# Kernel tuning notes

Hardware: AMD Instinct MI355X
Metric: run time of the kernel (lower is better)

## Reference

```python
import jax, jax.numpy as jnp
import numpy as np

N_LAYERS = 2
H = 16                      # num_heads
ARW = (1.0, 1.0)            # att_residual_weight
MCB = (0.0, 1.0)            # mask_clip_balancer
LN_EPS = 1e-5


def _ln(x, g, b):
    mu = jnp.mean(x, axis=-1, keepdims=True)
    var = jnp.mean(jnp.square(x - mu), axis=-1, keepdims=True)
    return (x - mu) * jax.lax.rsqrt(var + LN_EPS) * g + b


def _quick_gelu(u):
    return u * jax.nn.sigmoid(1.702 * u)


def setup_inputs() -> dict:
    key = jax.random.key(0)
    ks = jax.random.split(key, 8)
    L, B, C = 577, 8, 1024
    d_ff = 4 * C
    inp = {
        'x': jax.random.normal(ks[0], (L, B, C), jnp.float32),
        'att_bias': jax.random.normal(ks[1], (N_LAYERS, B * H, L, L), jnp.float32),
        'ln1_g': jnp.ones((N_LAYERS, C), jnp.float32),
        'ln1_b': jnp.zeros((N_LAYERS, C), jnp.float32),
        'in_w': 0.02 * jax.random.normal(ks[2], (N_LAYERS, 3 * C, C), jnp.float32),
        'in_b': jnp.zeros((N_LAYERS, 3 * C), jnp.float32),
        'out_w': 0.02 * jax.random.normal(ks[3], (N_LAYERS, C, C), jnp.float32),
        'out_b': jnp.zeros((N_LAYERS, C), jnp.float32),
        'ln2_g': jnp.ones((N_LAYERS, C), jnp.float32),
        'ln2_b': jnp.zeros((N_LAYERS, C), jnp.float32),
        'fc1_w': 0.02 * jax.random.normal(ks[4], (N_LAYERS, d_ff, C), jnp.float32),
        'fc1_b': jnp.zeros((N_LAYERS, d_ff), jnp.float32),
        'fc2_w': 0.02 * jax.random.normal(ks[5], (N_LAYERS, C, d_ff), jnp.float32),
        'fc2_b': jnp.zeros((N_LAYERS, C), jnp.float32),
    }
    return inp


def reference(x, att_bias, ln1_g, ln1_b, in_w, in_b, out_w, out_b,
              ln2_g, ln2_b, fc1_w, fc1_b, fc2_w, fc2_b):
    L, B, C = x.shape
    d = C // H
    scale = d ** -0.5  # custom_att_factor is None
    for i in range(N_LAYERS):
        # --- custom CSA attention ---
        h = _ln(x, ln1_g[i], ln1_b[i])                              # [L,B,C]
        qkv = jnp.einsum('lbc,fc->lbf', h, in_w[i]) + in_b[i]       # [L,B,3C]
        q, k, v = jnp.split(qkv, 3, axis=-1)
        to_heads = lambda t: t.reshape(L, B, H, d).transpose(1, 2, 0, 3)  # [B,H,L,d]
        q, k, v = to_heads(q), to_heads(k), to_heads(v)
        bias = att_bias[i].reshape(B, H, L, L)
        q_attn = bias + scale * jnp.einsum('bhld,bhmd->bhlm', q, q)
        k_attn = bias + scale * jnp.einsum('bhld,bhmd->bhlm', k, k)
        attn = jax.nn.softmax(q_attn, axis=-1) + jax.nn.softmax(k_attn, axis=-1)
        attn = attn * 0.5                                           # norm_att=True
        attn = jnp.mean(attn, axis=1, keepdims=True)                # avg_att=True -> [B,1,L,L]
        out = jnp.matmul(attn, v)                                   # broadcast over H -> [B,H,L,d]
        out = MCB[0] * v + MCB[1] * out
        out = out.transpose(2, 0, 1, 3).reshape(L, B, C)
        out = jnp.einsum('lbc,oc->lbo', out, out_w[i]) + out_b[i]
        x = ARW[0] * x + ARW[1] * out
        # --- MLP residual ---
        h2 = _ln(x, ln2_g[i], ln2_b[i])
        u = _quick_gelu(jnp.einsum('lbc,fc->lbf', h2, fc1_w[i]) + fc1_b[i])
        x = x + jnp.einsum('lbf,cf->lbc', u, fc2_w[i]) + fc2_b[i]
    return x
```

## Files before the change

kernel.cpp:

```cpp
#include <hip/hip_runtime.h>

typedef float f32x4 __attribute__((ext_vector_type(4)));
typedef __bf16 bf16x8 __attribute__((ext_vector_type(8)));

#define L_SEQ 577
#define BB 8
#define CC 1024
#define HH 16
#define ROWS (L_SEQ*BB)

static __device__ __forceinline__ ushort f2b(float f) {
  unsigned u = __float_as_uint(f);
  u += 0x7fffu + ((u >> 16) & 1u);
  return (ushort)(u >> 16);
}

static __device__ __forceinline__ void gld16(const void* g, void* l) {
  __builtin_amdgcn_global_load_lds((const __attribute__((address_space(1))) void*)g,
                                   (__attribute__((address_space(3))) void*)l, 16, 0, 0);
}

__global__ void cvt4_kernel(const float* __restrict__ s0, ushort* __restrict__ d0, int n0,
                            const float* __restrict__ s1, ushort* __restrict__ d1, int n1,
                            const float* __restrict__ s2, ushort* __restrict__ d2, int n2,
                            const float* __restrict__ s3, ushort* __restrict__ d3, int n3)
{
  int i = blockIdx.x * blockDim.x + threadIdx.x;
  const float* src; ushort* dst;
  if (i < n0)                { src = s0; dst = d0; }
  else if ((i -= n0) < n1)   { src = s1; dst = d1; }
  else if ((i -= n1) < n2)   { src = s2; dst = d2; }
  else if ((i -= n2) < n3)   { src = s3; dst = d3; }
  else return;
  float4 v = *(const float4*)(src + (size_t)i * 4);
  ushort4 o;
  o.x = f2b(v.x); o.y = f2b(v.y); o.z = f2b(v.z); o.w = f2b(v.w);
  *(ushort4*)(dst + (size_t)i * 4) = o;
}

template<int NP, bool DOLN>
__global__ __launch_bounds__(256)
void ln_resid_kernel(const float* __restrict__ xsrc, const float* __restrict__ parts,
                     const float* __restrict__ cbias,
                     const float* __restrict__ g, const float* __restrict__ be,
                     float* __restrict__ xdst, ushort* __restrict__ hout)
{
  const int row = blockIdx.x;
  const int t = threadIdx.x;
  float4 v = *(const float4*)(xsrc + (size_t)row * CC + t * 4);
  if (NP > 0) {
    float4 c4 = *(const float4*)(cbias + t * 4);
    v.x += c4.x; v.y += c4.y; v.z += c4.z; v.w += c4.w;
    #pragma unroll
    for (int p = 0; p < NP; ++p) {
      float4 pv = *(const float4*)(parts + ((size_t)p * ROWS + row) * CC + t * 4);
      v.x += pv.x; v.y += pv.y; v.z += pv.z; v.w += pv.w;
    }
  }
  *(float4*)(xdst + (size_t)row * CC + t * 4) = v;
  if (DOLN) {
    float s  = v.x + v.y + v.z + v.w;
    float s2 = v.x*v.x + v.y*v.y + v.z*v.z + v.w*v.w;
    #pragma unroll
    for (int sd = 1; sd < 64; sd <<= 1) { s += __shfl_xor(s, sd, 64); s2 += __shfl_xor(s2, sd, 64); }
    __shared__ float ps[4], ps2[4];
    const int w = t >> 6;
    if ((t & 63) == 0) { ps[w] = s; ps2[w] = s2; }
    __syncthreads();
    s  = ps[0] + ps[1] + ps[2] + ps[3];
    s2 = ps2[0] + ps2[1] + ps2[2] + ps2[3];
    const float mean = s * (1.f / 1024.f);
    const float var  = s2 * (1.f / 1024.f) - mean * mean;
    const float rstd = rsqrtf(var + 1e-5f);
    float4 gv = *(const float4*)(g + t * 4);
    float4 bv = *(const float4*)(be + t * 4);
    ushort4 o;
    o.x = f2b((v.x - mean) * rstd * gv.x + bv.x);
    o.y = f2b((v.y - mean) * rstd * gv.y + bv.y);
    o.z = f2b((v.z - mean) * rstd * gv.z + bv.z);
    o.w = f2b((v.w - mean) * rstd * gv.w + bv.w);
    *(ushort4*)(hout + (size_t)row * CC + t * 4) = o;
  }
}

__global__ __launch_bounds__(256)
void vt_kernel(const ushort* __restrict__ qkv, ushort* __restrict__ vt)
{
  __shared__ ushort tile[32][33];
  const int lt = blockIdx.x * 32;
  const int nt = blockIdx.y * 32;
  const int b  = blockIdx.z;
  const int tx = threadIdx.x & 31;
  const int ty = threadIdx.x >> 5;
  #pragma unroll
  for (int p = 0; p < 4; ++p) {
    int l = lt + ty + p * 8;
    ushort v = 0;
    if (l < L_SEQ) v = qkv[((size_t)l * BB + b) * 3072 + 2048 + nt + tx];
    tile[ty + p * 8][tx] = v;
  }
  __syncthreads();
  #pragma unroll
  for (int p = 0; p < 4; ++p) {
    int n = nt + ty + p * 8;
    int l = lt + tx;
    vt[((size_t)b * 1024 + n) * 608 + l] = tile[tx][ty + p * 8];
  }
}

__global__ __launch_bounds__(512, 2)
void attn_kernel(const ushort* __restrict__ qkv,
                 const float* __restrict__ bias,
                 ushort* __restrict__ attnp)
{
  __shared__ float2 red[2][2][8][16];
  __shared__ ushort sm[32][612];
  const int t = threadIdx.x;
  const int lane = t & 63;
  const int w = t >> 6;
  const int fr = lane & 15;
  const int lq = lane >> 4;
  const int id = blockIdx.x;
  const int b  = id & 7;
  const int rem = id >> 3;
  const int rb = rem % 19;
  const int hg = rem / 19;
  const int r0 = rb * 32;
  const int kc = lq * 8;

  int rowl[2]; size_t rbase[2];
  #pragma unroll
  for (int rs = 0; rs < 2; ++rs) {
    rowl[rs] = min(r0 + rs * 16 + fr, L_SEQ - 1);
    rbase[rs] = ((size_t)rowl[rs] * BB + b) * 3072;
  }
  size_t cbs_[5]; int c0_[5];
  #pragma unroll
  for (int it = 0; it < 5; ++it) {
    const int nt = w + it * 8;
    const int crow = min(nt * 16 + fr, L_SEQ - 1);
    cbs_[it] = ((size_t)crow * BB + b) * 3072;
    c0_[it] = nt * 16 + lq * 4;
  }

  float acc[2][5][4];
  #pragma unroll
  for (int rs = 0; rs < 2; ++rs)
    #pragma unroll
    for (int it = 0; it < 5; ++it)
      #pragma unroll
      for (int r = 0; r < 4; ++r) acc[rs][it][r] = 0.f;

  for (int h4 = 0; h4 < 4; ++h4) {
    const int h = hg * 4 + h4;
    const float* brow0 = bias + (((size_t)(b * HH + h)) * L_SEQ + rowl[0]) * L_SEQ;
    const float* brow1 = bias + (((size_t)(b * HH + h)) * L_SEQ + rowl[1]) * L_SEQ;
    float bs[2][5][4];
    #pragma unroll
    for (int it = 0; it < 5; ++it)
      #pragma unroll
      for (int r = 0; r < 4; ++r) {
        const int cc = min(c0_[it] + r, L_SEQ - 1);
        bs[0][it][r] = brow0[cc];
        bs[1][it][r] = brow1[cc];
      }
    #pragma unroll
    for (int v = 0; v < 2; ++v) {
      const int off = (v ? CC : 0) + h * 64;
      bf16x8 rf0[2], rf1[2];
      #pragma unroll
      for (int rs = 0; rs < 2; ++rs) {
        rf0[rs] = *(const bf16x8*)(qkv + rbase[rs] + off + kc);
        rf1[rs] = *(const bf16x8*)(qkv + rbase[rs] + off + 32 + kc);
      }
      bf16x8 cA0 = *(const bf16x8*)(qkv + cbs_[0] + off + kc);
      bf16x8 cA1 = *(const bf16x8*)(qkv + cbs_[0] + off + 32 + kc);
      bf16x8 cB0 = *(const bf16x8*)(qkv + cbs_[1] + off + kc);
      bf16x8 cB1 = *(const bf16x8*)(qkv + cbs_[1] + off + 32 + kc);
      float s[2][5][4];
      #pragma unroll
      for (int it = 0; it < 5; ++it) {
        const bf16x8 c0f = cA0, c1f = cA1;
        cA0 = cB0; cA1 = cB1;
        if (it + 2 < 5) {
          cB0 = *(const bf16x8*)(qkv + cbs_[it + 2] + off + kc);
          cB1 = *(const bf16x8*)(qkv + cbs_[it + 2] + off + 32 + kc);
        }
        f32x4 d0 = {0.f, 0.f, 0.f, 0.f};
        f32x4 d1 = {0.f, 0.f, 0.f, 0.f};
        d0 = __builtin_amdgcn_mfma_f32_16x16x32_bf16(c0f, rf0[0], d0, 0, 0, 0);
        d0 = __builtin_amdgcn_mfma_f32_16x16x32_bf16(c1f, rf1[0], d0, 0, 0, 0);
        d1 = __builtin_amdgcn_mfma_f32_16x16x32_bf16(c0f, rf0[1], d1, 0, 0, 0);
        d1 = __builtin_amdgcn_mfma_f32_16x16x32_bf16(c1f, rf1[1], d1, 0, 0, 0);
        #pragma unroll
        for (int r = 0; r < 4; ++r) {
          const bool cv = (c0_[it] + r < L_SEQ);
          s[0][it][r] = cv ? (bs[0][it][r] + 0.125f * d0[r]) : -1e30f;
          s[1][it][r] = cv ? (bs[1][it][r] + 0.125f * d1[r]) : -1e30f;
        }
      }
      float mw[2], sw[2];
      #pragma unroll
      for (int rs = 0; rs < 2; ++rs) {
        float m = -1e30f;
        #pragma unroll
        for (int it = 0; it < 5; ++it)
          #pragma unroll
          for (int r = 0; r < 4; ++r) m = fmaxf(m, s[rs][it][r]);
        m = fmaxf(m, __shfl_xor(m, 16, 64));
        m = fmaxf(m, __shfl_xor(m, 32, 64));
        float sum = 0.f;
        #pragma unroll
        for (int it = 0; it < 5; ++it)
          #pragma unroll
          for (int r = 0; r < 4; ++r) { s[rs][it][r] = __expf(s[rs][it][r] - m); sum += s[rs][it][r]; }
        sum += __shfl_xor(sum, 16, 64);
        sum += __shfl_xor(sum, 32, 64);
        mw[rs] = m; sw[rs] = sum;
      }
      const int p = (h4 * 2 + v) & 1;
      if (lane < 16) {
        red[p][0][w][lane] = make_float2(mw[0], sw[0]);
        red[p][1][w][lane] = make_float2(mw[1], sw[1]);
      }
      __syncthreads();
      #pragma unroll
      for (int rs = 0; rs < 2; ++rs) {
        float m = -1e30f;
        #pragma unroll
        for (int ww = 0; ww < 8; ++ww) m = fmaxf(m, red[p][rs][ww][fr].x);
        float smm = 0.f;
        #pragma unroll
        for (int ww = 0; ww < 8; ++ww) {
          const float2 q = red[p][rs][ww][fr];
          smm += q.y * __expf(q.x - m);
        }
        const float f = 0.03125f * __expf(mw[rs] - m) / smm;
        #pragma unroll
        for (int it = 0; it < 5; ++it)
          #pragma unroll
          for (int r = 0; r < 4; ++r) acc[rs][it][r] += s[rs][it][r] * f;
      }
    }
  }

  #pragma unroll
  for (int rs = 0; rs < 2; ++rs)
    #pragma unroll
    for (int it = 0; it < 5; ++it) {
      if (c0_[it] < 608) {
        ushort4 o;
        o.x = f2b(acc[rs][it][0]); o.y = f2b(acc[rs][it][1]);
        o.z = f2b(acc[rs][it][2]); o.w = f2b(acc[rs][it][3]);
        *(ushort4*)&sm[rs * 16 + fr][c0_[it]] = o;
      }
    }
  __syncthreads();
  ushort* dst = attnp + ((size_t)hg * 8 + b) * 608 * 608 + (size_t)r0 * 608;
  for (int j = t; j < 32 * 152; j += 512) {
    const int row = j / 152;
    const int c4 = (j % 152) * 4;
    if (r0 + row < L_SEQ)
      *(ushort4*)(dst + (size_t)row * 608 + c4) = *(const ushort4*)&sm[row][c4];
  }
}

__global__ __launch_bounds__(256)
void attn_combine(const ushort* __restrict__ attnp, ushort* __restrict__ attn)
{
  const int t = threadIdx.x;
  if (t >= 152) return;
  const int l = blockIdx.x;
  const int b = blockIdx.y;
  const int c0 = t * 4;
  const size_t base = ((size_t)b * 608 + l) * 608 + c0;
  const size_t hs = (size_t)8 * 608 * 608;
  float s[4] = {0.f, 0.f, 0.f, 0.f};
  #pragma unroll
  for (int p = 0; p < 4; ++p) {
    ushort4 v = *(const ushort4*)(attnp + p * hs + base);
    s[0] += __uint_as_float((unsigned)v.x << 16);
    s[1] += __uint_as_float((unsigned)v.y << 16);
    s[2] += __uint_as_float((unsigned)v.z << 16);
    s[3] += __uint_as_float((unsigned)v.w << 16);
  }
  ushort4 o;
  const bool lv = (l < L_SEQ);
  o.x = (lv && c0 + 0 < L_SEQ) ? f2b(s[0]) : (ushort)0;
  o.y = (lv && c0 + 1 < L_SEQ) ? f2b(s[1]) : (ushort)0;
  o.z = (lv && c0 + 2 < L_SEQ) ? f2b(s[2]) : (ushort)0;
  o.w = (lv && c0 + 3 < L_SEQ) ? f2b(s[3]) : (ushort)0;
  *(ushort4*)(attn + base) = o;
}

__global__ __launch_bounds__(256, 2)
void av_gemm(const ushort* __restrict__ A, int lda, int Arows, long aStride,
             const ushort* __restrict__ B, int ldb, long bStride,
             int M, int K,
             ushort* __restrict__ outb, int ldo)
{
  __shared__ __align__(16) ushort As[128 * 32];
  __shared__ __align__(16) ushort Bs[128 * 32];
  const int t = threadIdx.x;
  const int lane = t & 63;
  const int w = t >> 6;
  const int bm = blockIdx.x, bn = blockIdx.y, bz = blockIdx.z;
  const ushort* Ab = A + (long)bz * aStride;
  const ushort* Bb = B + (long)bz * bStride;
  const int srow = t >> 2;
  const int sc = (t & 3) * 8;
  const int wr = (w >> 1) * 64;
  const int wc = (w & 1) * 64;
  const int am1 = Arows - 1;
  f32x4 acc[4][4] = {};

  const int r0a = bm * 128 + srow;
  const int r0b = bn * 128 + srow;
  for (int kt = 0; kt < K; kt += 32) {
    __syncthreads();
    gld16(Ab + (size_t)min(r0a, am1) * lda + kt + sc, (void*)(As + t * 8));
    gld16(Ab + (size_t)min(r0a + 64, am1) * lda + kt + sc, (void*)(As + 2048 + t * 8));
    gld16(Bb + (size_t)r0b * ldb + kt + sc, (void*)(Bs + t * 8));
    gld16(Bb + (size_t)(r0b + 64) * ldb + kt + sc, (void*)(Bs + 2048 + t * 8));
    asm volatile("s_waitcnt vmcnt(0)" ::: "memory");
    __syncthreads();
    bf16x8 av[4], bv[4];
    const int fr = lane & 15;
    const int kc = (lane >> 4) * 8;
    #pragma unroll
    for (int m = 0; m < 4; ++m) av[m] = *(const bf16x8*)(As + (wr + m * 16 + fr) * 32 + kc);
    #pragma unroll
    for (int n = 0; n < 4; ++n) bv[n] = *(const bf16x8*)(Bs + (wc + n * 16 + fr) * 32 + kc);
    #pragma unroll
    for (int m = 0; m < 4; ++m)
      #pragma unroll
      for (int n = 0; n < 4; ++n)
        acc[m][n] = __builtin_amdgcn_mfma_f32_16x16x32_bf16(av[m], bv[n], acc[m][n], 0, 0, 0);
  }
  const int rbase = wr + (lane >> 4) * 4;
  const int cbase = wc + (lane & 15);
  #pragma unroll
  for (int n = 0; n < 4; ++n) {
    const int gn = bn * 128 + cbase + n * 16;
    #pragma unroll
    for (int m = 0; m < 4; ++m) {
      f32x4 d = acc[m][n];
      #pragma unroll
      for (int r = 0; r < 4; ++r) {
        const int gm = bm * 128 + rbase + m * 16 + r;
        if (gm < M) outb[((size_t)gm * 8 + bz) * ldo + gn] = f2b(d[r]);
      }
    }
  }
}

#define RD_A8(BOFS, MH) \
  _Pragma("unroll") for (int ks = 0; ks < 2; ++ks) \
  _Pragma("unroll") for (int m = 0; m < 4; ++m) \
    Af[ks][m] = rdA(BOFS, MH, ks, m);

#define RD_B4(BOFS, NH) \
  _Pragma("unroll") for (int ks = 0; ks < 2; ++ks) \
  _Pragma("unroll") for (int n = 0; n < 2; ++n) \
    Bf[NH][ks][n] = rdB(BOFS, NH, ks, n);

#define MFQ(MH, NH) \
  _Pragma("unroll") for (int ks = 0; ks < 2; ++ks) \
  _Pragma("unroll") for (int m = 0; m < 4; ++m) \
  _Pragma("unroll") for (int n = 0; n < 2; ++n) \
    acc[(MH)*4+m][(NH)*2+n] = __builtin_amdgcn_mfma_f32_16x16x32_bf16( \
        Af[ks][m], Bf[NH][ks][n], acc[(MH)*4+m][(NH)*2+n], 0, 0, 0);

#define BARO() \
  __builtin_amdgcn_sched_barrier(0); \
  __builtin_amdgcn_s_barrier(); \
  asm volatile("s_waitcnt lgkmcnt(0)" ::: "memory"); \
  __builtin_amdgcn_sched_barrier(0); \
  __builtin_amdgcn_s_setprio(1);

#define MF_END() \
  __builtin_amdgcn_s_setprio(0); \
  __builtin_amdgcn_sched_barrier(0); \
  __builtin_amdgcn_s_barrier();

template<int EPI>
__global__ __launch_bounds__(512, 2)
void gemm8(const ushort* __restrict__ Ap, int lda, int Arows,
           const ushort* __restrict__ Bp, int ldb,
           int M, int Ksplit,
           const float* __restrict__ bias,
           ushort* __restrict__ outb, float* __restrict__ outf, int ldo)
{
  __shared__ __align__(16) char smem[131072];
  const int t = threadIdx.x;
  const int lane = t & 63;
  const int w = t >> 6;
  const int wm = w >> 2, wn = w & 3;
  const int gx = gridDim.x;
  const int nwg = gx * gridDim.y;
  int id = blockIdx.y * gx + blockIdx.x;
  {
    const int q8 = nwg >> 3, r8 = nwg & 7;
    const int xcd = id & 7, pos = id >> 3;
    id = (xcd < r8 ? xcd * (q8 + 1) : r8 * (q8 + 1) + (xcd - r8) * q8) + pos;
  }
  const int bm = id % gx, bn = id / gx;
  const int bz = blockIdx.z;
  const int k0 = bz * Ksplit;
  const int iters = Ksplit >> 7;
  const int fr = lane & 15, lq = lane >> 4;

  f32x4 acc[8][4] = {};
  bf16x8 Af[2][4];
  bf16x8 Bf[2][2][2];

  const int rowj0 = t >> 3,        cbj0 = t & 7;
  const int rowj1 = (t + 512) >> 3, cbj1 = (t + 512) & 7;
  const ushort* pA[2][2]; const ushort* pB[2][2];
  #pragma unroll
  for (int h = 0; h < 2; ++h) {
    pA[h][0] = Ap + (size_t)min(bm*256 + h*128 + rowj0, Arows-1) * lda + k0 + ((cbj0 ^ (rowj0 & 7)) << 3);
    pA[h][1] = Ap + (size_t)min(bm*256 + h*128 + rowj1, Arows-1) * lda + k0 + ((cbj1 ^ (rowj1 & 7)) << 3);
    pB[h][0] = Bp + (size_t)(bn*256 + h*128 + rowj0) * ldb + k0 + ((cbj0 ^ (rowj0 & 7)) << 3);
    pB[h][1] = Bp + (size_t)(bn*256 + h*128 + rowj1) * ldb + k0 + ((cbj1 ^ (rowj1 & 7)) << 3);
  }

  auto stA = [&](int kt, int bofs, int h) {
    gld16(pA[h][0] + kt * 64, smem + bofs + h * 16384 + t * 16);
    gld16(pA[h][1] + kt * 64, smem + bofs + h * 16384 + (t + 512) * 16);
  };
  auto stB = [&](int kt, int bofs, int h) {
    gld16(pB[h][0] + kt * 64, smem + bofs + 32768 + h * 16384 + t * 16);
    gld16(pB[h][1] + kt * 64, smem + bofs + 32768 + h * 16384 + (t + 512) * 16);
  };
  auto rdA = [&](int bofs, int mh, int ks, int m) -> bf16x8 {
    const int rl = wm * 64 + m * 16 + fr;
    const int cb = (ks * 4 + lq) ^ (fr & 7);
    return *(const bf16x8*)(smem + bofs + mh * 16384 + rl * 128 + cb * 16);
  };
  auto rdB = [&](int bofs, int nh, int ks, int n) -> bf16x8 {
    const int rl = wn * 32 + n * 16 + fr;
    const int cb = (ks * 4 + lq) ^ (fr & 7);
    return *(const bf16x8*)(smem + bofs + 32768 + nh * 16384 + rl * 128 + cb * 16);
  };

  stA(0, 0, 0); stB(0, 0, 0); stB(0, 0, 1); stA(0, 0, 1);
  stA(1, 65536, 0); stB(1, 65536, 1); stA(1, 65536, 1);
  asm volatile("s_waitcnt vmcnt(6)" ::: "memory");
  __builtin_amdgcn_sched_barrier(0);
  __builtin_amdgcn_s_barrier();

  for (int i = 0; i < iters; ++i) {
    const bool more = (i + 1 < iters);
    const int kt2 = 2 * i + 2;
    RD_A8(0, 0) RD_B4(0, 0)
    stB(2 * i + 1, 65536, 0);
    BARO(); MFQ(0, 0) MF_END();
    RD_B4(0, 1)
    if (more) stA(kt2, 0, 0);
    BARO(); MFQ(0, 1) MF_END();
    RD_A8(0, 1)
    if (more) stB(kt2, 0, 1);
    BARO(); MFQ(1, 1) MF_END();
    if (more) stA(kt2, 0, 1);
    BARO(); MFQ(1, 0)
    __builtin_amdgcn_s_setprio(0);
    if (more) { asm volatile("s_waitcnt vmcnt(6)" ::: "memory"); }
    else      { asm volatile("s_waitcnt vmcnt(0)" ::: "memory"); }
    __builtin_amdgcn_sched_barrier(0);
    __builtin_amdgcn_s_barrier();
    RD_A8(65536, 0) RD_B4(65536, 0)
    if (more) stB(kt2, 0, 0);
    BARO(); MFQ(0, 0) MF_END();
    RD_B4(65536, 1)
    if (more) stA(2 * i + 3, 65536, 0);
    BARO(); MFQ(0, 1) MF_END();
    RD_A8(65536, 1)
    if (more) stB(2 * i + 3, 65536, 1);
    BARO(); MFQ(1, 1) MF_END();
    if (more) stA(2 * i + 3, 65536, 1);
    BARO(); MFQ(1, 0)
    __builtin_amdgcn_s_setprio(0);
    if (more) { asm volatile("s_waitcnt vmcnt(6)" ::: "memory"); }
    __builtin_amdgcn_sched_barrier(0);
    __builtin_amdgcn_s_barrier();
  }

  #pragma unroll
  for (int mh = 0; mh < 2; ++mh)
  #pragma unroll
  for (int nh = 0; nh < 2; ++nh)
  #pragma unroll
  for (int n = 0; n < 2; ++n) {
    const int gn = bn * 256 + nh * 128 + wn * 32 + n * 16 + fr;
    const float bval = (EPI == 4) ? 0.f : bias[gn];
    #pragma unroll
    for (int m = 0; m < 4; ++m) {
      f32x4 d = acc[mh * 4 + m][nh * 2 + n];
      #pragma unroll
      for (int r = 0; r < 4; ++r) {
        const int gm = bm * 256 + mh * 128 + wm * 64 + m * 16 + lq * 4 + r;
        if (gm < M) {
          if (EPI == 0) {
            outb[(size_t)gm * ldo + gn] = f2b(d[r] + bval);
          } else if (EPI == 1) {
            float v0 = d[r] + bval;
            outb[(size_t)gm * ldo + gn] = f2b(v0 / (1.f + __expf(-1.702f * v0)));
          } else {
            outf[((size_t)bz * M + gm) * ldo + gn] = d[r];
          }
        }
      }
    }
  }
}

extern "C" void kernel_launch(void* const* d_in, const int* in_sizes, int n_in,
                              void* d_out, int out_size, void* d_ws, size_t ws_size,
                              hipStream_t stream)
{
  (void)in_sizes; (void)n_in; (void)out_size; (void)ws_size;
  const float* x_in  = (const float*)d_in[0];
  const float* attb  = (const float*)d_in[1];
  const float* ln1_g = (const float*)d_in[2];
  const float* ln1_b = (const float*)d_in[3];
  const float* in_w  = (const float*)d_in[4];
  const float* in_b  = (const float*)d_in[5];
  const float* out_w = (const float*)d_in[6];
  const float* out_b = (const float*)d_in[7];
  const float* ln2_g = (const float*)d_in[8];
  const float* ln2_b = (const float*)d_in[9];
  const float* fc1_w = (const float*)d_in[10];
  const float* fc1_b = (const float*)d_in[11];
  const float* fc2_w = (const float*)d_in[12];
  const float* fc2_b = (const float*)d_in[13];
  float* x = (float*)d_out;

  char* ws = (char*)d_ws;
  size_t off = 0;
  auto alloc = [&](size_t bytes) -> void* {
    void* p = ws + off; off += (bytes + 255) & ~(size_t)255; return p;
  };
  ushort* wIn   = (ushort*)alloc(2ull * 3072 * 1024 * 2);
  ushort* wOut  = (ushort*)alloc(2ull * 1024 * 1024 * 2);
  ushort* wF1   = (ushort*)alloc(2ull * 4096 * 1024 * 2);
  ushort* wF2   = (ushort*)alloc(2ull * 4096 * 1024 * 2);
  ushort* hbuf  = (ushort*)alloc((size_t)ROWS * 1024 * 2);
  ushort* qkv   = (ushort*)alloc((size_t)ROWS * 3072 * 2);
  ushort* vt    = (ushort*)alloc((size_t)8 * 1024 * 608 * 2);
  ushort* attn  = (ushort*)alloc((size_t)8 * 608 * 608 * 2);
  ushort* attnp = (ushort*)alloc((size_t)4 * 8 * 608 * 608 * 2);
  ushort* outlb = (ushort*)alloc((size_t)ROWS * 1024 * 2);
  float*  pbuf  = (float*)alloc((size_t)4 * ROWS * 1024 * 4);
  ushort* ubuf  = qkv;

  cvt4_kernel<<<(1572864 + 524288 + 2097152 + 2097152 + 255) / 256, 256, 0, stream>>>(
      in_w,  wIn,  1572864,
      out_w, wOut, 524288,
      fc1_w, wF1,  2097152,
      fc2_w, wF2,  2097152);
  ln_resid_kernel<0, true><<<ROWS, 256, 0, stream>>>(x_in, nullptr, nullptr,
      ln1_g, ln1_b, x, hbuf);

  for (int i = 0; i < 2; ++i) {
    gemm8<0><<<dim3(19, 12, 1), 512, 0, stream>>>(hbuf, 1024, ROWS,
        wIn + (size_t)i * 3072 * 1024, 1024,
        ROWS, 1024, in_b + i * 3072, qkv, nullptr, 3072);
    attn_kernel<<<dim3(608, 1, 1), 512, 0, stream>>>(qkv, attb + (size_t)i * 128 * 577 * 577, attnp);
    vt_kernel<<<dim3(19, 32, 8), 256, 0, stream>>>(qkv, vt);
    attn_combine<<<dim3(608, 8), 256, 0, stream>>>(attnp, attn);
    av_gemm<<<dim3(5, 8, 8), 256, 0, stream>>>(attn, 608, 577, (long)608 * 608,
        vt, 608, (long)1024 * 608, 577, 608, outlb, 1024);
    gemm8<4><<<dim3(19, 4, 2), 512, 0, stream>>>(outlb, 1024, ROWS,
        wOut + (size_t)i * 1024 * 1024, 1024,
        ROWS, 512, nullptr, nullptr, pbuf, 1024);
    ln_resid_kernel<2, true><<<ROWS, 256, 0, stream>>>(x, pbuf, out_b + i * 1024,
        ln2_g + i * 1024, ln2_b + i * 1024, x, hbuf);
    gemm8<1><<<dim3(19, 16, 1), 512, 0, stream>>>(hbuf, 1024, ROWS,
        wF1 + (size_t)i * 4096 * 1024, 1024,
        ROWS, 1024, fc1_b + i * 4096, ubuf, nullptr, 4096);
    gemm8<4><<<dim3(19, 4, 4), 512, 0, stream>>>(ubuf, 4096, ROWS,
        wF2 + (size_t)i * 4096 * 1024, 4096,
        ROWS, 1024, nullptr, nullptr, pbuf, 1024);
    if (i == 0) {
      ln_resid_kernel<4, true><<<ROWS, 256, 0, stream>>>(x, pbuf, fc2_b,
          ln1_g + 1024, ln1_b + 1024, x, hbuf);
    } else {
      ln_resid_kernel<4, false><<<ROWS, 256, 0, stream>>>(x, pbuf, fc2_b + 1024,
          nullptr, nullptr, x, nullptr);
    }
  }
}
```

Before: 998.3 us.

## Write Q and K head-major from the QKV GEMM epilogue for the attention kernel

The QKV projection GEMM gets a new epilogue that scatters Q and K into padded per-(batch, head) buffers laid out as [b, h, L, 64], and writes V into its own [L*B, 1024] buffer. The attention kernel then reads each head's rows as contiguous 128-byte rows instead of gathering them at a 3072-element stride from the interleaved qkv tensor, which should improve cache-line use and locality. In exchange the GEMM epilogue does a per-element index computation and a scattered store. The workspace is reshuffled, and the MLP intermediate buffer now aliases the new Q buffer and spills into the buffers after it.

```diff
diff --git a/kernel.cpp b/kernel.cpp
--- a/kernel.cpp
+++ b/kernel.cpp
@@ -4,6 +4,7 @@
 typedef __bf16 bf16x8 __attribute__((ext_vector_type(8)));
 
 #define L_SEQ 577
+#define LPAD 584
 #define BB 8
 #define CC 1024
 #define HH 16
@@ -84,7 +85,7 @@
 }
 
 __global__ __launch_bounds__(256)
-void vt_kernel(const ushort* __restrict__ qkv, ushort* __restrict__ vt)
+void vt_kernel(const ushort* __restrict__ vbuf, ushort* __restrict__ vt)
 {
   __shared__ ushort tile[32][33];
   const int lt = blockIdx.x * 32;
@@ -96,7 +97,7 @@
   for (int p = 0; p < 4; ++p) {
     int l = lt + ty + p * 8;
     ushort v = 0;
-    if (l < L_SEQ) v = qkv[((size_t)l * BB + b) * 3072 + 2048 + nt + tx];
+    if (l < L_SEQ) v = vbuf[((size_t)l * BB + b) * 1024 + nt + tx];
     tile[ty + p * 8][tx] = v;
   }
   __syncthreads();
@@ -109,7 +110,7 @@
 }
 
 __global__ __launch_bounds__(512, 2)
-void attn_kernel(const ushort* __restrict__ qkv,
+void attn_kernel(const ushort* __restrict__ qh, const ushort* __restrict__ kh,
                  const float* __restrict__ bias,
                  ushort* __restrict__ attnp)
 {
@@ -128,18 +129,14 @@
   const int r0 = rb * 32;
   const int kc = lq * 8;
 
-  int rowl[2]; size_t rbase[2];
-  #pragma unroll
-  for (int rs = 0; rs < 2; ++rs) {
-    rowl[rs] = min(r0 + rs * 16 + fr, L_SEQ - 1);
-    rbase[rs] = ((size_t)rowl[rs] * BB + b) * 3072;
-  }
-  size_t cbs_[5]; int c0_[5];
+  int rowl[2];
+  #pragma unroll
+  for (int rs = 0; rs < 2; ++rs) rowl[rs] = min(r0 + rs * 16 + fr, L_SEQ - 1);
+  int crow_[5]; int c0_[5];
   #pragma unroll
   for (int it = 0; it < 5; ++it) {
     const int nt = w + it * 8;
-    const int crow = min(nt * 16 + fr, L_SEQ - 1);
-    cbs_[it] = ((size_t)crow * BB + b) * 3072;
+    crow_[it] = min(nt * 16 + fr, L_SEQ - 1);
     c0_[it] = nt * 16 + lq * 4;
   }
 
@@ -153,6 +150,7 @@
 
   for (int h4 = 0; h4 < 4; ++h4) {
     const int h = hg * 4 + h4;
+    const size_t hb = ((size_t)(b * 16 + h)) * LPAD * 64;
     const float* brow0 = bias + (((size_t)(b * HH + h)) * L_SEQ + rowl[0]) * L_SEQ;
     const float* brow1 = bias + (((size_t)(b * HH + h)) * L_SEQ + rowl[1]) * L_SEQ;
     float bs[2][5][4];
@@ -166,25 +164,25 @@
       }
     #pragma unroll
     for (int v = 0; v < 2; ++v) {
-      const int off = (v ? CC : 0) + h * 64;
+      const ushort* base = (v ? kh : qh) + hb;
       bf16x8 rf0[2], rf1[2];
       #pragma unroll
       for (int rs = 0; rs < 2; ++rs) {
-        rf0[rs] = *(const bf16x8*)(qkv + rbase[rs] + off + kc);
-        rf1[rs] = *(const bf16x8*)(qkv + rbase[rs] + off + 32 + kc);
-      }
-      bf16x8 cA0 = *(const bf16x8*)(qkv + cbs_[0] + off + kc);
-      bf16x8 cA1 = *(const bf16x8*)(qkv + cbs_[0] + off + 32 + kc);
-      bf16x8 cB0 = *(const bf16x8*)(qkv + cbs_[1] + off + kc);
-      bf16x8 cB1 = *(const bf16x8*)(qkv + cbs_[1] + off + 32 + kc);
+        rf0[rs] = *(const bf16x8*)(base + rowl[rs] * 64 + kc);
+        rf1[rs] = *(const bf16x8*)(base + rowl[rs] * 64 + 32 + kc);
+      }
+      bf16x8 cA0 = *(const bf16x8*)(base + crow_[0] * 64 + kc);
+      bf16x8 cA1 = *(const bf16x8*)(base + crow_[0] * 64 + 32 + kc);
+      bf16x8 cB0 = *(const bf16x8*)(base + crow_[1] * 64 + kc);
+      bf16x8 cB1 = *(const bf16x8*)(base + crow_[1] * 64 + 32 + kc);
       float s[2][5][4];
       #pragma unroll
       for (int it = 0; it < 5; ++it) {
         const bf16x8 c0f = cA0, c1f = cA1;
         cA0 = cB0; cA1 = cB1;
         if (it + 2 < 5) {
-          cB0 = *(const bf16x8*)(qkv + cbs_[it + 2] + off + kc);
-          cB1 = *(const bf16x8*)(qkv + cbs_[it + 2] + off + 32 + kc);
+          cB0 = *(const bf16x8*)(base + crow_[it + 2] * 64 + kc);
+          cB1 = *(const bf16x8*)(base + crow_[it + 2] * 64 + 32 + kc);
         }
         f32x4 d0 = {0.f, 0.f, 0.f, 0.f};
         f32x4 d1 = {0.f, 0.f, 0.f, 0.f};
@@ -389,7 +387,8 @@
            const ushort* __restrict__ Bp, int ldb,
            int M, int Ksplit,
            const float* __restrict__ bias,
-           ushort* __restrict__ outb, float* __restrict__ outf, int ldo)
+           ushort* __restrict__ outb, float* __restrict__ outf,
+           ushort* __restrict__ ob2, ushort* __restrict__ ob3, int ldo)
 {
   __shared__ __align__(16) char smem[131072];
   const int t = threadIdx.x;
@@ -496,18 +495,30 @@
     const float bval = (EPI == 4) ? 0.f : bias[gn];
     #pragma unroll
     for (int m = 0; m < 4; ++m) {
-      f32x4 d = acc[mh * 4 + m][nh * 2 + n];
+      f32x4 dv = acc[mh * 4 + m][nh * 2 + n];
       #pragma unroll
       for (int r = 0; r < 4; ++r) {
         const int gm = bm * 256 + mh * 128 + wm * 64 + m * 16 + lq * 4 + r;
         if (gm < M) {
           if (EPI == 0) {
-            outb[(size_t)gm * ldo + gn] = f2b(d[r] + bval);
+            outb[(size_t)gm * ldo + gn] = f2b(dv[r] + bval);
           } else if (EPI == 1) {
-            float v0 = d[r] + bval;
+            float v0 = dv[r] + bval;
             outb[(size_t)gm * ldo + gn] = f2b(v0 / (1.f + __expf(-1.702f * v0)));
+          } else if (EPI == 4) {
+            outf[((size_t)bz * M + gm) * ldo + gn] = dv[r];
           } else {
-            outf[((size_t)bz * M + gm) * ldo + gn] = d[r];
+            const int l = gm >> 3, bq = gm & 7;
+            const ushort val = f2b(dv[r] + bval);
+            if (gn < 1024) {
+              const int h = gn >> 6, d = gn & 63;
+              outb[(((size_t)(bq * 16 + h)) * LPAD + l) * 64 + d] = val;
+            } else if (gn < 2048) {
+              const int h = (gn - 1024) >> 6, d = gn & 63;
+              ob2[(((size_t)(bq * 16 + h)) * LPAD + l) * 64 + d] = val;
+            } else {
+              ob3[(size_t)gm * 1024 + (gn - 2048)] = val;
+            }
           }
         }
       }
@@ -546,13 +557,15 @@
   ushort* wF1   = (ushort*)alloc(2ull * 4096 * 1024 * 2);
   ushort* wF2   = (ushort*)alloc(2ull * 4096 * 1024 * 2);
   ushort* hbuf  = (ushort*)alloc((size_t)ROWS * 1024 * 2);
-  ushort* qkv   = (ushort*)alloc((size_t)ROWS * 3072 * 2);
+  ushort* qh    = (ushort*)alloc((size_t)8 * 16 * LPAD * 64 * 2);
+  ushort* kh    = (ushort*)alloc((size_t)8 * 16 * LPAD * 64 * 2);
+  ushort* vbuf  = (ushort*)alloc((size_t)ROWS * 1024 * 2);
   ushort* vt    = (ushort*)alloc((size_t)8 * 1024 * 608 * 2);
+  ushort* attnp = (ushort*)alloc((size_t)4 * 8 * 608 * 608 * 2);
   ushort* attn  = (ushort*)alloc((size_t)8 * 608 * 608 * 2);
-  ushort* attnp = (ushort*)alloc((size_t)4 * 8 * 608 * 608 * 2);
   ushort* outlb = (ushort*)alloc((size_t)ROWS * 1024 * 2);
   float*  pbuf  = (float*)alloc((size_t)4 * ROWS * 1024 * 4);
-  ushort* ubuf  = qkv;
+  ushort* ubuf  = qh;
 
   cvt4_kernel<<<(1572864 + 524288 + 2097152 + 2097152 + 255) / 256, 256, 0, stream>>>(
       in_w,  wIn,  1572864,
@@ -563,25 +576,26 @@
       ln1_g, ln1_b, x, hbuf);
 
   for (int i = 0; i < 2; ++i) {
-    gemm8<0><<<dim3(19, 12, 1), 512, 0, stream>>>(hbuf, 1024, ROWS,
+    gemm8<5><<<dim3(19, 12, 1), 512, 0, stream>>>(hbuf, 1024, ROWS,
         wIn + (size_t)i * 3072 * 1024, 1024,
-        ROWS, 1024, in_b + i * 3072, qkv, nullptr, 3072);
-    attn_kernel<<<dim3(608, 1, 1), 512, 0, stream>>>(qkv, attb + (size_t)i * 128 * 577 * 577, attnp);
-    vt_kernel<<<dim3(19, 32, 8), 256, 0, stream>>>(qkv, vt);
+        ROWS, 1024, in_b + i * 3072, qh, nullptr, kh, vbuf, 3072);
+    attn_kernel<<<dim3(608, 1, 1), 512, 0, stream>>>(qh, kh,
+        attb + (size_t)i * 128 * 577 * 577, attnp);
+    vt_kernel<<<dim3(19, 32, 8), 256, 0, stream>>>(vbuf, vt);
     attn_combine<<<dim3(608, 8), 256, 0, stream>>>(attnp, attn);
     av_gemm<<<dim3(5, 8, 8), 256, 0, stream>>>(attn, 608, 577, (long)608 * 608,
         vt, 608, (long)1024 * 608, 577, 608, outlb, 1024);
     gemm8<4><<<dim3(19, 4, 2), 512, 0, stream>>>(outlb, 1024, ROWS,
         wOut + (size_t)i * 1024 * 1024, 1024,
-        ROWS, 512, nullptr, nullptr, pbuf, 1024);
+        ROWS, 512, nullptr, nullptr, pbuf, nullptr, nullptr, 1024);
     ln_resid_kernel<2, true><<<ROWS, 256, 0, stream>>>(x, pbuf, out_b + i * 1024,
         ln2_g + i * 1024, ln2_b + i * 1024, x, hbuf);
     gemm8<1><<<dim3(19, 16, 1), 512, 0, stream>>>(hbuf, 1024, ROWS,
         wF1 + (size_t)i * 4096 * 1024, 1024,
-        ROWS, 1024, fc1_b + i * 4096, ubuf, nullptr, 4096);
+        ROWS, 1024, fc1_b + i * 4096, ubuf, nullptr, nullptr, nullptr, 4096);
     gemm8<4><<<dim3(19, 4, 4), 512, 0, stream>>>(ubuf, 4096, ROWS,
         wF2 + (size_t)i * 4096 * 1024, 4096,
-        ROWS, 1024, nullptr, nullptr, pbuf, 1024);
+        ROWS, 1024, nullptr, nullptr, pbuf, nullptr, nullptr, 1024);
     if (i == 0) {
       ln_resid_kernel<4, true><<<ROWS, 256, 0, stream>>>(x, pbuf, fc2_b,
           ln1_g + 1024, ln1_b + 1024, x, hbuf);
```

Result: slower. 1.065 ms (+6.6%).
